# Kernel tuning notes

Hardware: AMD Instinct MI355X
Metric: run time of the kernel (lower is better)

Reference implementation:

```python
import jax, jax.numpy as jnp
import numpy as np

B, T, D = 4, 2048, 1024
H = 16
HD = D // H  # 64

def setup_inputs() -> dict:
    key = jax.random.key(0)
    ks = jax.random.split(key, 5)
    x = jax.random.normal(ks[0], (B, T, D), dtype=jnp.float32)
    # Linear params, torch default init scale ~ U(-1/sqrt(fan_in), 1/sqrt(fan_in))
    s = 1.0 / np.sqrt(D)
    W_qkv = jax.random.uniform(ks[1], (D, 3 * D), jnp.float32, -s, s)
    b_qkv = jax.random.uniform(ks[2], (3 * D,), jnp.float32, -s, s)
    W_proj = jax.random.uniform(ks[3], (D, D), jnp.float32, -s, s)
    b_proj = jax.random.uniform(ks[4], (D,), jnp.float32, -s, s)
    return {"x": x, "W_qkv": W_qkv, "b_qkv": b_qkv, "W_proj": W_proj, "b_proj": b_proj}

def reference(x, W_qkv, b_qkv, W_proj, b_proj):
    b, t, c = x.shape
    qkv = x @ W_qkv + b_qkv                       # [B,T,3D]
    q, k, v = jnp.split(qkv, 3, axis=-1)
    # [B,T,D] -> [B,H,T,HD]
    def heads(a):
        return a.reshape(b, t, H, HD).transpose(0, 2, 1, 3)
    q, k, v = heads(q), heads(k), heads(v)
    scale = 1.0 / jnp.sqrt(jnp.float32(HD))
    att = jnp.einsum('bhqd,bhkd->bhqk', q, k) * scale   # [B,H,T,T]
    causal = jnp.tril(jnp.ones((t, t), dtype=bool))
    att = jnp.where(causal, att, -jnp.inf)
    att = jax.nn.softmax(att, axis=-1)
    out = jnp.einsum('bhqk,bhkd->bhqd', att, v)          # [B,H,T,HD]
    out = out.transpose(0, 2, 1, 3).reshape(b, t, c)
    return out @ W_proj + b_proj
```

## Files before the change

### kernel.cpp

```cpp
#include <hip/hip_runtime.h>
#include <hip/hip_bf16.h>
#include <stdint.h>

using u16 = unsigned short;
using u32t = unsigned int;
typedef __bf16 bf16x8 __attribute__((ext_vector_type(8)));
typedef float f32x4 __attribute__((ext_vector_type(4)));
typedef float f32x16 __attribute__((ext_vector_type(16)));

#define SEQ_T 2048
#define DM 1024
#define NH 16
#define HD 64
#define NB 4

__device__ inline u16 f2bfu(float f) {
    __hip_bfloat16 h = __float2bfloat16(f);
    return __builtin_bit_cast(u16, h);
}

__device__ inline bf16x8 ld_frag(const u16* p) {
    return __builtin_bit_cast(bf16x8, *reinterpret_cast<const uint4*>(p));
}

__device__ inline void gload_lds16(const u16* g, u16* l) {
    __builtin_amdgcn_global_load_lds(
        (const __attribute__((address_space(1))) void*)g,
        (__attribute__((address_space(3))) void*)l, 16, 0, 0);
}

__device__ inline float fexp2(float x) { return __builtin_amdgcn_exp2f(x); }

__global__ __launch_bounds__(256) void cvt_x_kernel(const float* __restrict__ x,
                                                    u16* __restrict__ o) {
    size_t i = (size_t)blockIdx.x * 256 + threadIdx.x;
    const float4* xv = reinterpret_cast<const float4*>(x);
    float4 a = xv[2 * i];
    float4 b = xv[2 * i + 1];
    u16 r[8] = {f2bfu(a.x), f2bfu(a.y), f2bfu(a.z), f2bfu(a.w),
                f2bfu(b.x), f2bfu(b.y), f2bfu(b.z), f2bfu(b.w)};
    *reinterpret_cast<uint4*>(o + i * 8) = *reinterpret_cast<const uint4*>(r);
}

__global__ __launch_bounds__(256) void trans_w(const float* __restrict__ W,
                                               u16* __restrict__ Wt,
                                               int K, int N) {
    __shared__ __align__(16) float tile[64][72];
    int k0 = blockIdx.y * 64, n0 = blockIdx.x * 64;
    int tid = threadIdx.x;
#pragma unroll
    for (int p = 0; p < 4; ++p) {
        int idx = p * 256 + tid;
        int r = idx >> 4, c = (idx & 15) * 4;
        float4 v = *reinterpret_cast<const float4*>(&W[(size_t)(k0 + r) * N + n0 + c]);
        *reinterpret_cast<float4*>(&tile[r][c]) = v;
    }
    __syncthreads();
#pragma unroll
    for (int p = 0; p < 4; ++p) {
        int idx = p * 256 + tid;
        int nr = idx >> 4, kg = (idx & 15) * 4;
        u16 u[4];
#pragma unroll
        for (int j = 0; j < 4; ++j) u[j] = f2bfu(tile[kg + j][nr]);
        *reinterpret_cast<uint2*>(&Wt[(size_t)(n0 + nr) * K + k0 + kg]) =
            *reinterpret_cast<const uint2*>(u);
    }
}

template <int F32OUT, int SCALEQ>
__global__ __launch_bounds__(512, 2) void gemm_r3(const u16* __restrict__ A,
                                                  const u16* __restrict__ Bt,
                                                  const float* __restrict__ bias,
                                                  float* __restrict__ Cf,
                                                  u16* __restrict__ Cb,
                                                  int M, int N, int K) {
    __shared__ __align__(16) u16 smem[36864];
    const int tid = threadIdx.x;
    const int wid = tid >> 6, lane = tid & 63;
    const int llo = lane & 15, lhi = lane >> 4;
    const int wm = wid >> 1, wn = wid & 1;
    const int cpx = gridDim.x >> 3;
    const int swz = (blockIdx.x & 7) * cpx + (blockIdx.x >> 3);
    const int nb = N >> 7;
    const int m0 = (swz / nb) << 8, n0 = (swz % nb) << 7;
    const int T = K >> 5;

    f32x4 acc[4][4];
#pragma unroll
    for (int i = 0; i < 4; ++i)
#pragma unroll
        for (int j = 0; j < 4; ++j) acc[i][j] = (f32x4){0.f, 0.f, 0.f, 0.f};

    auto stage = [&](int t, int sb) {
        const int kb = t << 5;
#pragma unroll
        for (int j = 0; j < 2; ++j) {
            int c = j * 512 + tid;
            int row = c >> 2, kc = (c & 3) * 8;
            gload_lds16(A + (size_t)(m0 + row) * K + kb + kc, smem + sb + c * 8);
        }
        {
            int c = tid;
            int row = c >> 2, kc = (c & 3) * 8;
            gload_lds16(Bt + (size_t)(n0 + row) * K + kb + kc,
                        smem + sb + 8192 + c * 8);
        }
    };

    stage(0, 0);
    stage(1, 12288);

    for (int t = 0; t < T; ++t) {
        if (t == T - 1)
            asm volatile("s_waitcnt vmcnt(0)" ::: "memory");
        else
            asm volatile("s_waitcnt vmcnt(3)" ::: "memory");
        __builtin_amdgcn_sched_barrier(0);
        __builtin_amdgcn_s_barrier();
        __builtin_amdgcn_sched_barrier(0);
        const u16* Ab = smem + (t % 3) * 12288;
        const u16* Bb = Ab + 8192;
        bf16x8 af[4], bfr[4];
#pragma unroll
        for (int mf = 0; mf < 4; ++mf)
            af[mf] = ld_frag(Ab + (wm * 64 + mf * 16 + llo) * 32 + lhi * 8);
#pragma unroll
        for (int nf = 0; nf < 4; ++nf)
            bfr[nf] = ld_frag(Bb + (wn * 64 + nf * 16 + llo) * 32 + lhi * 8);
        if (t + 2 < T) stage(t + 2, ((t + 2) % 3) * 12288);
        __builtin_amdgcn_s_setprio(1);
#pragma unroll
        for (int mf = 0; mf < 4; ++mf)
#pragma unroll
            for (int nf = 0; nf < 4; ++nf)
                acc[mf][nf] = __builtin_amdgcn_mfma_f32_16x16x32_bf16(
                    af[mf], bfr[nf], acc[mf][nf], 0, 0, 0);
        __builtin_amdgcn_s_setprio(0);
    }

    const float SC2 = 0.18033688f;
    const int row_base = m0 + wm * 64;
    const int col_base = n0 + wn * 64;
#pragma unroll
    for (int nf = 0; nf < 4; ++nf) {
        int col = col_base + nf * 16 + llo;
        float bv = bias[col];
        const bool doScale = SCALEQ && (col < 1024);
#pragma unroll
        for (int mf = 0; mf < 4; ++mf) {
#pragma unroll
            for (int r = 0; r < 4; ++r) {
                int row = row_base + mf * 16 + lhi * 4 + r;
                float v = acc[mf][nf][r] + bv;
                if (doScale) v *= SC2;
                if (F32OUT)
                    Cf[(size_t)row * N + col] = v;
                else
                    Cb[(size_t)row * N + col] = f2bfu(v);
            }
        }
    }
}

template <int F32OUT, int SCALEQ>
__global__ __launch_bounds__(256, 3) void gemm_r4(const u16* __restrict__ A,
                                                  const u16* __restrict__ Bt,
                                                  const float* __restrict__ bias,
                                                  float* __restrict__ Cf,
                                                  u16* __restrict__ Cb,
                                                  int M, int N, int K) {
    __shared__ __align__(16) u16 smem[24576];
    const int tid = threadIdx.x;
    const int wid = tid >> 6, lane = tid & 63;
    const int llo = lane & 15, lhi = lane >> 4;
    const int wm = wid >> 1, wn = wid & 1;
    const int cpx = gridDim.x >> 3;
    const int swz = (blockIdx.x & 7) * cpx + (blockIdx.x >> 3);
    const int nb = N >> 7;
    const int m0 = (swz / nb) << 7, n0 = (swz % nb) << 7;
    const int T = K >> 5;

    f32x4 acc[4][4];
#pragma unroll
    for (int i = 0; i < 4; ++i)
#pragma unroll
        for (int j = 0; j < 4; ++j) acc[i][j] = (f32x4){0.f, 0.f, 0.f, 0.f};

    auto stage = [&](int t, int sb) {
        const int kb = t << 5;
#pragma unroll
        for (int j = 0; j < 2; ++j) {
            int c = j * 256 + tid;
            int row = c >> 2, kc = (c & 3) * 8;
            gload_lds16(A + (size_t)(m0 + row) * K + kb + kc, smem + sb + c * 8);
        }
#pragma unroll
        for (int j = 0; j < 2; ++j) {
            int c = j * 256 + tid;
            int row = c >> 2, kc = (c & 3) * 8;
            gload_lds16(Bt + (size_t)(n0 + row) * K + kb + kc,
                        smem + sb + 4096 + c * 8);
        }
    };

    stage(0, 0);
    stage(1, 8192);

    for (int t = 0; t < T; ++t) {
        if (t == T - 1)
            asm volatile("s_waitcnt vmcnt(0)" ::: "memory");
        else
            asm volatile("s_waitcnt vmcnt(4)" ::: "memory");
        __builtin_amdgcn_sched_barrier(0);
        __builtin_amdgcn_s_barrier();
        __builtin_amdgcn_sched_barrier(0);
        const u16* Ab = smem + (t % 3) * 8192;
        const u16* Bb = Ab + 4096;
        bf16x8 af[4], bfr[4];
#pragma unroll
        for (int mf = 0; mf < 4; ++mf)
            af[mf] = ld_frag(Ab + (wm * 64 + mf * 16 + llo) * 32 + lhi * 8);
#pragma unroll
        for (int nf = 0; nf < 4; ++nf)
            bfr[nf] = ld_frag(Bb + (wn * 64 + nf * 16 + llo) * 32 + lhi * 8);
        if (t + 2 < T) stage(t + 2, ((t + 2) % 3) * 8192);
        __builtin_amdgcn_s_setprio(1);
#pragma unroll
        for (int mf = 0; mf < 4; ++mf)
#pragma unroll
            for (int nf = 0; nf < 4; ++nf)
                acc[mf][nf] = __builtin_amdgcn_mfma_f32_16x16x32_bf16(
                    af[mf], bfr[nf], acc[mf][nf], 0, 0, 0);
        __builtin_amdgcn_s_setprio(0);
    }

    const float SC2 = 0.18033688f;
    const int row_base = m0 + wm * 64;
    const int col_base = n0 + wn * 64;
#pragma unroll
    for (int nf = 0; nf < 4; ++nf) {
        int col = col_base + nf * 16 + llo;
        float bv = bias[col];
        const bool doScale = SCALEQ && (col < 1024);
#pragma unroll
        for (int mf = 0; mf < 4; ++mf) {
#pragma unroll
            for (int r = 0; r < 4; ++r) {
                int row = row_base + mf * 16 + lhi * 4 + r;
                float v = acc[mf][nf][r] + bv;
                if (doScale) v *= SC2;
                if (F32OUT)
                    Cf[(size_t)row * N + col] = v;
                else
                    Cb[(size_t)row * N + col] = f2bfu(v);
            }
        }
    }
}

__global__ __launch_bounds__(512, 2) void attn_kernel(const u16* __restrict__ qkv,
                                                      u16* __restrict__ o) {
    __shared__ __align__(16) u16 smem[34048];
    const int bid = blockIdx.x;
    const int amap[8] = {7, 5, 3, 1, 6, 4, 2, 0};
    const int bh = bid & 63;
    const int qc = amap[bid >> 6];
    const int b = bh >> 4, h = bh & 15;
    const int tid = threadIdx.x;
    const int wid = tid >> 6, lane = tid & 63;
    const int l31 = lane & 31, lh = lane >> 5;
    const u16* base = qkv + (size_t)b * SEQ_T * (3 * DM);
    const int qrow0 = qc * 256 + wid * 32;
    const int q_abs = qrow0 + l31;
    const int nkv2 = 2 * qc + 2;

    bf16x8 qf[4];
    {
        const u16* qp = base + (size_t)q_abs * (3 * DM) + h * HD + lh * 8;
#pragma unroll
        for (int km = 0; km < 4; ++km) qf[km] = ld_frag(qp + km * 16);
    }

    f32x16 oac0, oac1;
#pragma unroll
    for (int r = 0; r < 16; ++r) { oac0[r] = 0.f; oac1[r] = 0.f; }
    float m_run = -1e30f, l_run = 0.f;

    uint4 va, vb;
    const int vpr = tid >> 3, vm = tid & 7;

    auto stageK = [&](int kb2, int bi2) {
#pragma unroll
        for (int p = 0; p < 2; ++p) {
            int kv = p * 64 + wid * 8 + (lane >> 3);
            int cl = lane & 7;
            const u16* src = base + (size_t)(kb2 * 128 + kv) * (3 * DM) + DM + h * HD +
                             ((cl ^ (kv & 7)) * 8);
            gload_lds16(src, smem + bi2 * 8320 + (p * 8 + wid) * 520);
        }
    };
    auto loadV = [&](int kb2) {
        const u16* vp =
            base + (size_t)(kb2 * 128 + 2 * vpr) * (3 * DM) + 2 * DM + h * HD + vm * 8;
        va = *reinterpret_cast<const uint4*>(vp);
        vb = *reinterpret_cast<const uint4*>(vp + 3 * DM);
    };
    auto writeV = [&](int bi2) {
        u16 ua[8], ub[8];
        *reinterpret_cast<uint4*>(ua) = va;
        *reinterpret_cast<uint4*>(ub) = vb;
        const int cbk = vpr >> 2, off = 2 * (vpr & 3);
        const int sw = (2 * vm) & 7;
        u16* vt = smem + 16640 + bi2 * 8704;
#pragma unroll
        for (int j = 0; j < 8; ++j) {
            int d = vm * 8 + j;
            u32t val = (u32t)ua[j] | ((u32t)ub[j] << 16);
            *reinterpret_cast<u32t*>(vt + d * 136 + ((cbk ^ sw) * 8) + off) = val;
        }
    };

    loadV(0);
    stageK(0, 0);
    writeV(0);
    asm volatile("s_waitcnt lgkmcnt(0)" ::: "memory");
    asm volatile("s_waitcnt vmcnt(1)" ::: "memory");
    __builtin_amdgcn_sched_barrier(0);
    __builtin_amdgcn_s_barrier();
    __builtin_amdgcn_sched_barrier(0);

    const int vsw = (2 * (l31 >> 3)) & 7;
    const int qmax = qrow0 + 31;
    const int krow0 = (l31 >> 3) * 520 + (l31 & 7) * 64;
    const int krow1 = (4 + (l31 >> 3)) * 520 + (l31 & 7) * 64;

    for (int kb2 = 0; kb2 < nkv2; ++kb2) {
        const int cur = kb2 & 1;
        const bool pre = (kb2 + 1 < nkv2);
        if (pre) { loadV(kb2 + 1); stageK(kb2 + 1, cur ^ 1); }

#pragma unroll
        for (int s = 0; s < 2; ++s) {
            if (s == 1) {
                if (pre) asm volatile("s_waitcnt vmcnt(4)" ::: "memory");
                else     asm volatile("s_waitcnt vmcnt(0)" ::: "memory");
                __builtin_amdgcn_sched_barrier(0);
            }
            const int kv0 = kb2 * 128 + s * 64;
            if (kv0 > qmax) continue;
            f32x16 s0, s1;
#pragma unroll
            for (int r = 0; r < 16; ++r) { s0[r] = 0.f; s1[r] = 0.f; }
            const u16* kbase = smem + cur * 8320 + s * 4160;
#pragma unroll
            for (int km = 0; km < 4; ++km) {
                bf16x8 kf = ld_frag(kbase + krow0 + (((km * 2 + lh) ^ (l31 & 7)) * 8));
                s0 = __builtin_amdgcn_mfma_f32_32x32x16_bf16(kf, qf[km], s0, 0, 0, 0);
            }
#pragma unroll
            for (int km = 0; km < 4; ++km) {
                bf16x8 kf = ld_frag(kbase + krow1 + (((km * 2 + lh) ^ (l31 & 7)) * 8));
                s1 = __builtin_amdgcn_mfma_f32_32x32x16_bf16(kf, qf[km], s1, 0, 0, 0);
            }

            if (kv0 + 63 > qrow0) {
#pragma unroll
                for (int r = 0; r < 16; ++r) {
                    int ka = kv0 + (r & 3) + 8 * (r >> 2) + 4 * lh;
                    if (ka > q_abs) s0[r] = -1e30f;
                    if (ka + 32 > q_abs) s1[r] = -1e30f;
                }
            }

            float t16[16];
#pragma unroll
            for (int r = 0; r < 16; ++r) t16[r] = fmaxf(s0[r], s1[r]);
#pragma unroll
            for (int r = 0; r < 8; ++r) t16[r] = fmaxf(t16[r], t16[r + 8]);
#pragma unroll
            for (int r = 0; r < 4; ++r) t16[r] = fmaxf(t16[r], t16[r + 4]);
            float pm = fmaxf(fmaxf(t16[0], t16[1]), fmaxf(t16[2], t16[3]));
            pm = fmaxf(pm, __shfl_xor(pm, 32));
            if (!__all(pm - m_run <= 8.f)) {
                const float mnew = fmaxf(m_run, pm);
                const float sc = fexp2(m_run - mnew);
                m_run = mnew;
                l_run *= sc;
#pragma unroll
                for (int r = 0; r < 16; ++r) { oac0[r] *= sc; oac1[r] *= sc; }
            }
            float a16[16];
#pragma unroll
            for (int r = 0; r < 16; ++r) { s0[r] = fexp2(s0[r] - m_run); }
#pragma unroll
            for (int r = 0; r < 16; ++r) { s1[r] = fexp2(s1[r] - m_run); }
#pragma unroll
            for (int r = 0; r < 16; ++r) a16[r] = s0[r] + s1[r];
#pragma unroll
            for (int r = 0; r < 8; ++r) a16[r] += a16[r + 8];
#pragma unroll
            for (int r = 0; r < 4; ++r) a16[r] += a16[r + 4];
            float sum = (a16[0] + a16[1]) + (a16[2] + a16[3]);
            sum += __shfl_xor(sum, 32);
            l_run += sum;

            u32t pk0[8], pk1[8];
#pragma unroll
            for (int w = 0; w < 8; ++w) {
                float a0 = s0[2 * w], b0 = s0[2 * w + 1];
                float a1 = s1[2 * w], b1 = s1[2 * w + 1];
                asm("v_cvt_pk_bf16_f32 %0, %1, %2" : "=v"(pk0[w]) : "v"(a0), "v"(b0));
                asm("v_cvt_pk_bf16_f32 %0, %1, %2" : "=v"(pk1[w]) : "v"(a1), "v"(b1));
            }
            asm("v_permlane32_swap_b32 %0, %1" : "+v"(pk0[0]), "+v"(pk0[2]));
            asm("v_permlane32_swap_b32 %0, %1" : "+v"(pk0[1]), "+v"(pk0[3]));
            asm("v_permlane32_swap_b32 %0, %1" : "+v"(pk0[4]), "+v"(pk0[6]));
            asm("v_permlane32_swap_b32 %0, %1" : "+v"(pk0[5]), "+v"(pk0[7]));
            asm("v_permlane32_swap_b32 %0, %1" : "+v"(pk1[0]), "+v"(pk1[2]));
            asm("v_permlane32_swap_b32 %0, %1" : "+v"(pk1[1]), "+v"(pk1[3]));
            asm("v_permlane32_swap_b32 %0, %1" : "+v"(pk1[4]), "+v"(pk1[6]));
            asm("v_permlane32_swap_b32 %0, %1" : "+v"(pk1[5]), "+v"(pk1[7]));
            bf16x8 pf[4];
            {
                uint4 t0 = {pk0[0], pk0[1], pk0[2], pk0[3]};
                uint4 t1 = {pk0[4], pk0[5], pk0[6], pk0[7]};
                uint4 t2 = {pk1[0], pk1[1], pk1[2], pk1[3]};
                uint4 t3 = {pk1[4], pk1[5], pk1[6], pk1[7]};
                pf[0] = __builtin_bit_cast(bf16x8, t0);
                pf[1] = __builtin_bit_cast(bf16x8, t1);
                pf[2] = __builtin_bit_cast(bf16x8, t2);
                pf[3] = __builtin_bit_cast(bf16x8, t3);
            }

            const u16* vbase = smem + 16640 + cur * 8704;
#pragma unroll
            for (int km = 0; km < 4; ++km) {
                bf16x8 vf = ld_frag(vbase + l31 * 136 +
                                    ((s * 8 + ((km * 2 + lh) ^ vsw)) * 8));
                oac0 = __builtin_amdgcn_mfma_f32_32x32x16_bf16(vf, pf[km], oac0, 0, 0, 0);
            }
#pragma unroll
            for (int km = 0; km < 4; ++km) {
                bf16x8 vf = ld_frag(vbase + (32 + l31) * 136 +
                                    ((s * 8 + ((km * 2 + lh) ^ vsw)) * 8));
                oac1 = __builtin_amdgcn_mfma_f32_32x32x16_bf16(vf, pf[km], oac1, 0, 0, 0);
            }
        }

        if (pre) {
            writeV(cur ^ 1);
            asm volatile("s_waitcnt lgkmcnt(0)" ::: "memory");
            asm volatile("s_waitcnt vmcnt(1)" ::: "memory");
        } else {
            asm volatile("s_waitcnt lgkmcnt(0)" ::: "memory");
        }
        __builtin_amdgcn_sched_barrier(0);
        __builtin_amdgcn_s_barrier();
        __builtin_amdgcn_sched_barrier(0);
    }

    const float inv = 1.f / l_run;
    u16* osh = smem + wid * 2240;
#pragma unroll
    for (int r = 0; r < 16; ++r) {
        int dl = (r & 3) + 8 * (r >> 2) + 4 * lh;
        osh[l31 * 70 + dl] = f2bfu(oac0[r] * inv);
        osh[l31 * 70 + 32 + dl] = f2bfu(oac1[r] * inv);
    }
    __syncthreads();
    {
        const u16* rs = osh + l31 * 70 + lh * 32;
        u16* op = o + (size_t)(b * SEQ_T + qrow0 + l31) * DM + h * HD + lh * 32;
        u32t w[16];
#pragma unroll
        for (int i = 0; i < 16; ++i) w[i] = *reinterpret_cast<const u32t*>(rs + i * 2);
#pragma unroll
        for (int i = 0; i < 4; ++i) {
            uint4 t = {w[4 * i], w[4 * i + 1], w[4 * i + 2], w[4 * i + 3]};
            *reinterpret_cast<uint4*>(op + 8 * i) = t;
        }
    }
}

extern "C" void kernel_launch(void* const* d_in, const int* in_sizes, int n_in,
                              void* d_out, int out_size, void* d_ws, size_t ws_size,
                              hipStream_t stream) {
    const float* x = (const float*)d_in[0];
    const float* Wqkv = (const float*)d_in[1];
    const float* bqkv = (const float*)d_in[2];
    const float* Wproj = (const float*)d_in[3];
    const float* bproj = (const float*)d_in[4];
    float* out = (float*)d_out;
    char* ws = (char*)d_ws;

    u16* xb   = (u16*)(ws);
    u16* wtq  = (u16*)(ws + 16777216);
    u16* wtp  = (u16*)(ws + 23068672);
    u16* qkvb = (u16*)(ws + 25165824);
    u16* ob   = (u16*)(ws + 75497472);

    cvt_x_kernel<<<4096, 256, 0, stream>>>(x, xb);
    trans_w<<<dim3(3072 / 64, 1024 / 64), 256, 0, stream>>>(Wqkv, wtq, 1024, 3072);
    trans_w<<<dim3(1024 / 64, 1024 / 64), 256, 0, stream>>>(Wproj, wtp, 1024, 1024);

    gemm_r3<0, 1><<<768, 512, 0, stream>>>(
        xb, wtq, bqkv, nullptr, qkvb, 8192, 3072, 1024);

    attn_kernel<<<512, 512, 0, stream>>>(qkvb, ob);

    gemm_r4<1, 0><<<512, 256, 0, stream>>>(
        ob, wtp, bproj, out, nullptr, 8192, 1024, 1024);
}
```

Before: 162.5 us.

## Merge prep kernels into one launch and issue both QK^T halves before softmax

```diff
diff --git a/kernel.cpp b/kernel.cpp
--- a/kernel.cpp
+++ b/kernel.cpp
@@ -31,23 +31,36 @@
 
 __device__ inline float fexp2(float x) { return __builtin_amdgcn_exp2f(x); }
 
-__global__ __launch_bounds__(256) void cvt_x_kernel(const float* __restrict__ x,
-                                                    u16* __restrict__ o) {
-    size_t i = (size_t)blockIdx.x * 256 + threadIdx.x;
-    const float4* xv = reinterpret_cast<const float4*>(x);
-    float4 a = xv[2 * i];
-    float4 b = xv[2 * i + 1];
-    u16 r[8] = {f2bfu(a.x), f2bfu(a.y), f2bfu(a.z), f2bfu(a.w),
-                f2bfu(b.x), f2bfu(b.y), f2bfu(b.z), f2bfu(b.w)};
-    *reinterpret_cast<uint4*>(o + i * 8) = *reinterpret_cast<const uint4*>(r);
-}
-
-__global__ __launch_bounds__(256) void trans_w(const float* __restrict__ W,
-                                               u16* __restrict__ Wt,
-                                               int K, int N) {
+__global__ __launch_bounds__(256) void prep_kernel(const float* __restrict__ x,
+                                                   u16* __restrict__ xb,
+                                                   const float* __restrict__ Wqkv,
+                                                   u16* __restrict__ wtq,
+                                                   const float* __restrict__ Wproj,
+                                                   u16* __restrict__ wtp) {
     __shared__ __align__(16) float tile[64][72];
-    int k0 = blockIdx.y * 64, n0 = blockIdx.x * 64;
-    int tid = threadIdx.x;
+    const int bid = blockIdx.x;
+    const int tid = threadIdx.x;
+    if (bid < 4096) {
+        size_t i = (size_t)bid * 256 + tid;
+        const float4* xv = reinterpret_cast<const float4*>(x);
+        float4 a = xv[2 * i];
+        float4 b = xv[2 * i + 1];
+        u16 r[8] = {f2bfu(a.x), f2bfu(a.y), f2bfu(a.z), f2bfu(a.w),
+                    f2bfu(b.x), f2bfu(b.y), f2bfu(b.z), f2bfu(b.w)};
+        *reinterpret_cast<uint4*>(xb + i * 8) = *reinterpret_cast<const uint4*>(r);
+        return;
+    }
+    const float* W;
+    u16* Wt;
+    int N, t;
+    if (bid < 4864) {
+        W = Wqkv; Wt = wtq; N = 3072; t = bid - 4096;
+    } else {
+        W = Wproj; Wt = wtp; N = 1024; t = bid - 4864;
+    }
+    const int nbx = N >> 6;
+    const int n0 = (t % nbx) * 64, k0 = (t / nbx) * 64;
+    const int K = 1024;
 #pragma unroll
     for (int p = 0; p < 4; ++p) {
         int idx = p * 256 + tid;
@@ -340,42 +353,65 @@
         const bool pre = (kb2 + 1 < nkv2);
         if (pre) { loadV(kb2 + 1); stageK(kb2 + 1, cur ^ 1); }
 
-#pragma unroll
-        for (int s = 0; s < 2; ++s) {
-            if (s == 1) {
-                if (pre) asm volatile("s_waitcnt vmcnt(4)" ::: "memory");
-                else     asm volatile("s_waitcnt vmcnt(0)" ::: "memory");
-                __builtin_amdgcn_sched_barrier(0);
-            }
-            const int kv0 = kb2 * 128 + s * 64;
-            if (kv0 > qmax) continue;
-            f32x16 s0, s1;
-#pragma unroll
-            for (int r = 0; r < 16; ++r) { s0[r] = 0.f; s1[r] = 0.f; }
-            const u16* kbase = smem + cur * 8320 + s * 4160;
+        const int kv0A = kb2 * 128, kv0B = kv0A + 64;
+        const bool runA = (kv0A <= qmax), runB = (kv0B <= qmax);
+        f32x16 sA0, sA1, sB0, sB1;
+
+        if (runA) {
+#pragma unroll
+            for (int r = 0; r < 16; ++r) { sA0[r] = 0.f; sA1[r] = 0.f; }
+            const u16* kbase = smem + cur * 8320;
 #pragma unroll
             for (int km = 0; km < 4; ++km) {
                 bf16x8 kf = ld_frag(kbase + krow0 + (((km * 2 + lh) ^ (l31 & 7)) * 8));
-                s0 = __builtin_amdgcn_mfma_f32_32x32x16_bf16(kf, qf[km], s0, 0, 0, 0);
+                sA0 = __builtin_amdgcn_mfma_f32_32x32x16_bf16(kf, qf[km], sA0, 0, 0, 0);
             }
 #pragma unroll
             for (int km = 0; km < 4; ++km) {
                 bf16x8 kf = ld_frag(kbase + krow1 + (((km * 2 + lh) ^ (l31 & 7)) * 8));
-                s1 = __builtin_amdgcn_mfma_f32_32x32x16_bf16(kf, qf[km], s1, 0, 0, 0);
-            }
-
-            if (kv0 + 63 > qrow0) {
+                sA1 = __builtin_amdgcn_mfma_f32_32x32x16_bf16(kf, qf[km], sA1, 0, 0, 0);
+            }
+            if (kv0A + 63 > qrow0) {
 #pragma unroll
                 for (int r = 0; r < 16; ++r) {
-                    int ka = kv0 + (r & 3) + 8 * (r >> 2) + 4 * lh;
-                    if (ka > q_abs) s0[r] = -1e30f;
-                    if (ka + 32 > q_abs) s1[r] = -1e30f;
+                    int ka = kv0A + (r & 3) + 8 * (r >> 2) + 4 * lh;
+                    if (ka > q_abs) sA0[r] = -1e30f;
+                    if (ka + 32 > q_abs) sA1[r] = -1e30f;
                 }
             }
-
+        }
+
+        if (pre) asm volatile("s_waitcnt vmcnt(4)" ::: "memory");
+        else     asm volatile("s_waitcnt vmcnt(0)" ::: "memory");
+        __builtin_amdgcn_sched_barrier(0);
+        if (runB) {
+#pragma unroll
+            for (int r = 0; r < 16; ++r) { sB0[r] = 0.f; sB1[r] = 0.f; }
+            const u16* kbase = smem + cur * 8320 + 4160;
+#pragma unroll
+            for (int km = 0; km < 4; ++km) {
+                bf16x8 kf = ld_frag(kbase + krow0 + (((km * 2 + lh) ^ (l31 & 7)) * 8));
+                sB0 = __builtin_amdgcn_mfma_f32_32x32x16_bf16(kf, qf[km], sB0, 0, 0, 0);
+            }
+#pragma unroll
+            for (int km = 0; km < 4; ++km) {
+                bf16x8 kf = ld_frag(kbase + krow1 + (((km * 2 + lh) ^ (l31 & 7)) * 8));
+                sB1 = __builtin_amdgcn_mfma_f32_32x32x16_bf16(kf, qf[km], sB1, 0, 0, 0);
+            }
+            if (kv0B + 63 > qrow0) {
+#pragma unroll
+                for (int r = 0; r < 16; ++r) {
+                    int ka = kv0B + (r & 3) + 8 * (r >> 2) + 4 * lh;
+                    if (ka > q_abs) sB0[r] = -1e30f;
+                    if (ka + 32 > q_abs) sB1[r] = -1e30f;
+                }
+            }
+        }
+
+        if (runA) {
             float t16[16];
 #pragma unroll
-            for (int r = 0; r < 16; ++r) t16[r] = fmaxf(s0[r], s1[r]);
+            for (int r = 0; r < 16; ++r) t16[r] = fmaxf(sA0[r], sA1[r]);
 #pragma unroll
             for (int r = 0; r < 8; ++r) t16[r] = fmaxf(t16[r], t16[r + 8]);
 #pragma unroll
@@ -392,11 +428,11 @@
             }
             float a16[16];
 #pragma unroll
-            for (int r = 0; r < 16; ++r) { s0[r] = fexp2(s0[r] - m_run); }
-#pragma unroll
-            for (int r = 0; r < 16; ++r) { s1[r] = fexp2(s1[r] - m_run); }
-#pragma unroll
-            for (int r = 0; r < 16; ++r) a16[r] = s0[r] + s1[r];
+            for (int r = 0; r < 16; ++r) { sA0[r] = fexp2(sA0[r] - m_run); }
+#pragma unroll
+            for (int r = 0; r < 16; ++r) { sA1[r] = fexp2(sA1[r] - m_run); }
+#pragma unroll
+            for (int r = 0; r < 16; ++r) a16[r] = sA0[r] + sA1[r];
 #pragma unroll
             for (int r = 0; r < 8; ++r) a16[r] += a16[r + 8];
 #pragma unroll
@@ -408,8 +444,8 @@
             u32t pk0[8], pk1[8];
 #pragma unroll
             for (int w = 0; w < 8; ++w) {
-                float a0 = s0[2 * w], b0 = s0[2 * w + 1];
-                float a1 = s1[2 * w], b1 = s1[2 * w + 1];
+                float a0 = sA0[2 * w], b0 = sA0[2 * w + 1];
+                float a1 = sA1[2 * w], b1 = sA1[2 * w + 1];
                 asm("v_cvt_pk_bf16_f32 %0, %1, %2" : "=v"(pk0[w]) : "v"(a0), "v"(b0));
                 asm("v_cvt_pk_bf16_f32 %0, %1, %2" : "=v"(pk1[w]) : "v"(a1), "v"(b1));
             }
@@ -432,18 +468,88 @@
                 pf[2] = __builtin_bit_cast(bf16x8, t2);
                 pf[3] = __builtin_bit_cast(bf16x8, t3);
             }
-
             const u16* vbase = smem + 16640 + cur * 8704;
 #pragma unroll
             for (int km = 0; km < 4; ++km) {
-                bf16x8 vf = ld_frag(vbase + l31 * 136 +
-                                    ((s * 8 + ((km * 2 + lh) ^ vsw)) * 8));
+                bf16x8 vf = ld_frag(vbase + l31 * 136 + (((km * 2 + lh) ^ vsw) * 8));
                 oac0 = __builtin_amdgcn_mfma_f32_32x32x16_bf16(vf, pf[km], oac0, 0, 0, 0);
             }
 #pragma unroll
             for (int km = 0; km < 4; ++km) {
-                bf16x8 vf = ld_frag(vbase + (32 + l31) * 136 +
-                                    ((s * 8 + ((km * 2 + lh) ^ vsw)) * 8));
+                bf16x8 vf = ld_frag(vbase + (32 + l31) * 136 + (((km * 2 + lh) ^ vsw) * 8));
+                oac1 = __builtin_amdgcn_mfma_f32_32x32x16_bf16(vf, pf[km], oac1, 0, 0, 0);
+            }
+        }
+
+        if (runB) {
+            float t16[16];
+#pragma unroll
+            for (int r = 0; r < 16; ++r) t16[r] = fmaxf(sB0[r], sB1[r]);
+#pragma unroll
+            for (int r = 0; r < 8; ++r) t16[r] = fmaxf(t16[r], t16[r + 8]);
+#pragma unroll
+            for (int r = 0; r < 4; ++r) t16[r] = fmaxf(t16[r], t16[r + 4]);
+            float pm = fmaxf(fmaxf(t16[0], t16[1]), fmaxf(t16[2], t16[3]));
+            pm = fmaxf(pm, __shfl_xor(pm, 32));
+            if (!__all(pm - m_run <= 8.f)) {
+                const float mnew = fmaxf(m_run, pm);
+                const float sc = fexp2(m_run - mnew);
+                m_run = mnew;
+                l_run *= sc;
+#pragma unroll
+                for (int r = 0; r < 16; ++r) { oac0[r] *= sc; oac1[r] *= sc; }
+            }
+            float a16[16];
+#pragma unroll
+            for (int r = 0; r < 16; ++r) { sB0[r] = fexp2(sB0[r] - m_run); }
+#pragma unroll
+            for (int r = 0; r < 16; ++r) { sB1[r] = fexp2(sB1[r] - m_run); }
+#pragma unroll
+            for (int r = 0; r < 16; ++r) a16[r] = sB0[r] + sB1[r];
+#pragma unroll
+            for (int r = 0; r < 8; ++r) a16[r] += a16[r + 8];
+#pragma unroll
+            for (int r = 0; r < 4; ++r) a16[r] += a16[r + 4];
+            float sum = (a16[0] + a16[1]) + (a16[2] + a16[3]);
+            sum += __shfl_xor(sum, 32);
+            l_run += sum;
+
+            u32t pk0[8], pk1[8];
+#pragma unroll
+            for (int w = 0; w < 8; ++w) {
+                float a0 = sB0[2 * w], b0 = sB0[2 * w + 1];
+                float a1 = sB1[2 * w], b1 = sB1[2 * w + 1];
+                asm("v_cvt_pk_bf16_f32 %0, %1, %2" : "=v"(pk0[w]) : "v"(a0), "v"(b0));
+                asm("v_cvt_pk_bf16_f32 %0, %1, %2" : "=v"(pk1[w]) : "v"(a1), "v"(b1));
+            }
+            asm("v_permlane32_swap_b32 %0, %1" : "+v"(pk0[0]), "+v"(pk0[2]));
+            asm("v_permlane32_swap_b32 %0, %1" : "+v"(pk0[1]), "+v"(pk0[3]));
+            asm("v_permlane32_swap_b32 %0, %1" : "+v"(pk0[4]), "+v"(pk0[6]));
+            asm("v_permlane32_swap_b32 %0, %1" : "+v"(pk0[5]), "+v"(pk0[7]));
+            asm("v_permlane32_swap_b32 %0, %1" : "+v"(pk1[0]), "+v"(pk1[2]));
+            asm("v_permlane32_swap_b32 %0, %1" : "+v"(pk1[1]), "+v"(pk1[3]));
+            asm("v_permlane32_swap_b32 %0, %1" : "+v"(pk1[4]), "+v"(pk1[6]));
+            asm("v_permlane32_swap_b32 %0, %1" : "+v"(pk1[5]), "+v"(pk1[7]));
+            bf16x8 pf[4];
+            {
+                uint4 t0 = {pk0[0], pk0[1], pk0[2], pk0[3]};
+                uint4 t1 = {pk0[4], pk0[5], pk0[6], pk0[7]};
+                uint4 t2 = {pk1[0], pk1[1], pk1[2], pk1[3]};
+                uint4 t3 = {pk1[4], pk1[5], pk1[6], pk1[7]};
+                pf[0] = __builtin_bit_cast(bf16x8, t0);
+                pf[1] = __builtin_bit_cast(bf16x8, t1);
+                pf[2] = __builtin_bit_cast(bf16x8, t2);
+                pf[3] = __builtin_bit_cast(bf16x8, t3);
+            }
+            const u16* vbase = smem + 16640 + cur * 8704;
+#pragma unroll
+            for (int km = 0; km < 4; ++km) {
+                bf16x8 vf = ld_frag(vbase + l31 * 136 + ((8 + ((km * 2 + lh) ^ vsw)) * 8));
+                oac0 = __builtin_amdgcn_mfma_f32_32x32x16_bf16(vf, pf[km], oac0, 0, 0, 0);
+            }
+#pragma unroll
+            for (int km = 0; km < 4; ++km) {
+                bf16x8 vf = ld_frag(vbase + (32 + l31) * 136 + ((8 + ((km * 2 + lh) ^ vsw)) * 8));
                 oac1 = __builtin_amdgcn_mfma_f32_32x32x16_bf16(vf, pf[km], oac1, 0, 0, 0);
             }
         }
@@ -500,9 +606,7 @@
     u16* qkvb = (u16*)(ws + 25165824);
     u16* ob   = (u16*)(ws + 75497472);
 
-    cvt_x_kernel<<<4096, 256, 0, stream>>>(x, xb);
-    trans_w<<<dim3(3072 / 64, 1024 / 64), 256, 0, stream>>>(Wqkv, wtq, 1024, 3072);
-    trans_w<<<dim3(1024 / 64, 1024 / 64), 256, 0, stream>>>(Wproj, wtp, 1024, 1024);
+    prep_kernel<<<5120, 256, 0, stream>>>(x, xb, Wqkv, wtq, Wproj, wtp);
 
     gemm_r3<0, 1><<<768, 512, 0, stream>>>(
         xb, wtq, bqkv, nullptr, qkvb, 8192, 3072, 1024);
```

Measured after the change: 166.2 us. +2.3%, slower.
